# Optimization experiments

Hardware: AMD Instinct MI355X
Metric: run time of the kernel (lower is better)

Reference implementation:

```python
import jax, jax.numpy as jnp
import numpy as np
from jax import lax

B, T, C = 256, 128, 512
HID, HOR = 1024, 96
THR = 1.0


def setup_inputs() -> dict:
    key = jax.random.key(0)
    ks = jax.random.split(key, 6)
    x = jax.random.normal(ks[0], (B, T, C), dtype=jnp.float32)
    # fc1: Linear(C -> HID), PyTorch layout [out, in]
    W1 = jax.random.normal(ks[1], (HID, C), dtype=jnp.float32) / np.sqrt(C)
    b1 = jax.random.normal(ks[2], (HID,), dtype=jnp.float32) * 0.01
    # head: Linear(HID -> HOR)
    Wh = jax.random.normal(ks[3], (HOR, HID), dtype=jnp.float32) / np.sqrt(HID)
    bh = jax.random.normal(ks[4], (HOR,), dtype=jnp.float32) * 0.01
    beta = jnp.float32(0.9)  # learnable leak (snntorch Leaky, learn_beta=True)
    return {"x": x, "W1": W1, "b1": b1, "Wh": Wh, "bh": bh, "beta": beta}


def reference(x, W1, b1, Wh, bh, beta):
    # Precompute all fc1 projections as one batched GEMM: [B,T,HID]
    proj = jnp.einsum("btc,hc->bth", x, W1) + b1
    beta_c = jnp.clip(beta, 0.0, 1.0)

    def step(mem, inp):
        # snntorch Leaky, reset_mechanism='subtract': reset based on PREVIOUS mem
        reset = (mem > THR).astype(mem.dtype)  # detached in snntorch
        mem_new = beta_c * mem + inp - reset * THR
        return mem_new, None

    mem0 = jnp.zeros((x.shape[0], W1.shape[0]), dtype=x.dtype)
    mem_T, _ = lax.scan(step, mem0, jnp.moveaxis(proj, 1, 0))  # scan over T
    return mem_T @ Wh.T + bh  # [B, HOR]
```

## Files before the change

kernel.cpp:

```cpp
#include <hip/hip_runtime.h>

#define TT 128
#define CC 512
#define HIDN 1024
#define HORN 96
#define NB 256
#define BM 128
#define BN 256
#define BK 32
#define NSTAGE 16

typedef _Float16 f16x8 __attribute__((ext_vector_type(8)));
typedef _Float16 f16x4 __attribute__((ext_vector_type(4)));
typedef float f32x16 __attribute__((ext_vector_type(16)));

#define BUFSZ 49152
#define WOFF  16384
#define SMEM_BYTES 98304

__device__ __forceinline__ void cvt_split(const float4 v, f16x4* hi, f16x4* lo) {
    auto h01 = __builtin_amdgcn_cvt_pkrtz(v.x, v.y);
    auto h23 = __builtin_amdgcn_cvt_pkrtz(v.z, v.w);
    auto l01 = __builtin_amdgcn_cvt_pkrtz(v.x - (float)h01.x, v.y - (float)h01.y);
    auto l23 = __builtin_amdgcn_cvt_pkrtz(v.z - (float)h23.x, v.w - (float)h23.y);
    *hi = (f16x4){(_Float16)h01.x, (_Float16)h01.y, (_Float16)h23.x, (_Float16)h23.y};
    *lo = (f16x4){(_Float16)l01.x, (_Float16)l01.y, (_Float16)l23.x, (_Float16)l23.y};
}

__device__ __forceinline__ void cvt_split8(const float4 f0, const float4 f1,
                                           f16x8* hi, f16x8* lo) {
    auto h0 = __builtin_amdgcn_cvt_pkrtz(f0.x, f0.y);
    auto h1 = __builtin_amdgcn_cvt_pkrtz(f0.z, f0.w);
    auto h2 = __builtin_amdgcn_cvt_pkrtz(f1.x, f1.y);
    auto h3 = __builtin_amdgcn_cvt_pkrtz(f1.z, f1.w);
    auto l0 = __builtin_amdgcn_cvt_pkrtz(f0.x - (float)h0.x, f0.y - (float)h0.y);
    auto l1 = __builtin_amdgcn_cvt_pkrtz(f0.z - (float)h1.x, f0.w - (float)h1.y);
    auto l2 = __builtin_amdgcn_cvt_pkrtz(f1.x - (float)h2.x, f1.y - (float)h2.y);
    auto l3 = __builtin_amdgcn_cvt_pkrtz(f1.z - (float)h3.x, f1.w - (float)h3.y);
    *hi = (f16x8){(_Float16)h0.x, (_Float16)h0.y, (_Float16)h1.x, (_Float16)h1.y,
                  (_Float16)h2.x, (_Float16)h2.y, (_Float16)h3.x, (_Float16)h3.y};
    *lo = (f16x8){(_Float16)l0.x, (_Float16)l0.y, (_Float16)l1.x, (_Float16)l1.y,
                  (_Float16)l2.x, (_Float16)l2.y, (_Float16)l3.x, (_Float16)l3.y};
}

__device__ __forceinline__ void gload16(const void* g, void* l) {
    __builtin_amdgcn_global_load_lds(
        (const __attribute__((address_space(1))) unsigned int*)g,
        (__attribute__((address_space(3))) unsigned int*)l, 16, 0, 0);
}

__global__ void __launch_bounds__(256)
snn_cvtw(const float* __restrict__ W1, f16x4* __restrict__ whi, f16x4* __restrict__ wlo,
         const float* __restrict__ bh, float* __restrict__ out)
{
    const int i = blockIdx.x * 256 + threadIdx.x;
    const float4 v = ((const float4*)W1)[i];
    f16x4 hi, lo;
    cvt_split(v, &hi, &lo);
    whi[i] = hi;
    wlo[i] = lo;
    if (i < NB * HORN) out[i] = bh[i % HORN];
}

__global__ void __launch_bounds__(512, 1)
snn_proj_scan(const float* __restrict__ x, const _Float16* __restrict__ whi_g,
              const _Float16* __restrict__ wlo_g, const float* __restrict__ b1,
              const float* __restrict__ betap, float* __restrict__ memT)
{
    __shared__ __align__(16) char smem[SMEM_BYTES];

    const int tid  = threadIdx.x;
    const int lane = tid & 63;
    const int wid  = tid >> 6;
    const int wm = wid >> 2, wn = wid & 3;
    const int g2 = lane >> 5, lr = lane & 31;
    const int am = lr & 7;

    const int lid = blockIdx.x;
    const int idx = lid >> 3;
    const int b     = ((lid & 7) << 5) + (idx >> 2);
    const int hbase = (idx & 3) * BN;

    const int rr = lane >> 3, pp = lane & 7;
    const int uu = pp ^ rr;
    const char* xgc = (const char*)(x + (size_t)b * TT * CC);
    const char* xsrc0 = xgc + (size_t)(16 * wid + rr) * 2048 + uu * 16;
    const char* xsrc1 = xgc + (size_t)(16 * wid + 8 + rr) * 2048 + uu * 16;
    const char* wbase = (uu < 4) ? (const char*)whi_g : (const char*)wlo_g;
    const char* wsrc0 = wbase + (size_t)(hbase + 32 * wid + rr) * 1024 + (uu & 3) * 16;
    const char* wsrc1 = wsrc0 + 8 * 1024;
    const char* wsrc2 = wsrc0 + 16 * 1024;
    const char* wsrc3 = wsrc0 + 24 * 1024;

    const int arow0 = (wm * 64 + lr) * 128;
    const int arow1 = arow0 + 32 * 128;
    const int brow0 = WOFF + (wn * 64 + lr) * 128;
    const int brow1 = brow0 + 32 * 128;

    f32x16 acc00 = {}, acc01 = {}, acc10 = {}, acc11 = {};

#define STAGE_LOADS(S, BB) { \
        gload16(xsrc0 + (S) * 128, smem + (BB) + (2 * wid) * 1024); \
        gload16(xsrc1 + (S) * 128, smem + (BB) + (2 * wid + 1) * 1024); \
        gload16(wsrc0 + (S) * 64,  smem + (BB) + WOFF + (4 * wid) * 1024); \
        gload16(wsrc1 + (S) * 64,  smem + (BB) + WOFF + (4 * wid + 1) * 1024); \
        gload16(wsrc2 + (S) * 64,  smem + (BB) + WOFF + (4 * wid + 2) * 1024); \
        gload16(wsrc3 + (S) * 64,  smem + (BB) + WOFF + (4 * wid + 3) * 1024); }

#define KSTEP(CUR, KS) { \
        const int ua16 = (((KS) * 4 + g2 * 2) ^ am) << 4; \
        const int ub16 = (((KS) * 2 + g2) ^ am) << 4; \
        const float4 a00 = *(const float4*)(smem + (CUR) + arow0 + ua16); \
        const float4 a01 = *(const float4*)(smem + (CUR) + arow0 + (ua16 ^ 16)); \
        const float4 a10 = *(const float4*)(smem + (CUR) + arow1 + ua16); \
        const float4 a11 = *(const float4*)(smem + (CUR) + arow1 + (ua16 ^ 16)); \
        const f16x8 bh0 = *(const f16x8*)(smem + (CUR) + brow0 + ub16); \
        const f16x8 bl0 = *(const f16x8*)(smem + (CUR) + brow0 + (ub16 ^ 64)); \
        const f16x8 bh1 = *(const f16x8*)(smem + (CUR) + brow1 + ub16); \
        const f16x8 bl1 = *(const f16x8*)(smem + (CUR) + brow1 + (ub16 ^ 64)); \
        f16x8 ah0, al0, ah1, al1; \
        cvt_split8(a00, a01, &ah0, &al0); \
        cvt_split8(a10, a11, &ah1, &al1); \
        acc00 = __builtin_amdgcn_mfma_f32_32x32x16_f16(ah0, bh0, acc00, 0, 0, 0); \
        acc01 = __builtin_amdgcn_mfma_f32_32x32x16_f16(ah0, bh1, acc01, 0, 0, 0); \
        acc10 = __builtin_amdgcn_mfma_f32_32x32x16_f16(ah1, bh0, acc10, 0, 0, 0); \
        acc11 = __builtin_amdgcn_mfma_f32_32x32x16_f16(ah1, bh1, acc11, 0, 0, 0); \
        acc00 = __builtin_amdgcn_mfma_f32_32x32x16_f16(ah0, bl0, acc00, 0, 0, 0); \
        acc01 = __builtin_amdgcn_mfma_f32_32x32x16_f16(ah0, bl1, acc01, 0, 0, 0); \
        acc10 = __builtin_amdgcn_mfma_f32_32x32x16_f16(ah1, bl0, acc10, 0, 0, 0); \
        acc11 = __builtin_amdgcn_mfma_f32_32x32x16_f16(ah1, bl1, acc11, 0, 0, 0); \
        acc00 = __builtin_amdgcn_mfma_f32_32x32x16_f16(al0, bh0, acc00, 0, 0, 0); \
        acc01 = __builtin_amdgcn_mfma_f32_32x32x16_f16(al0, bh1, acc01, 0, 0, 0); \
        acc10 = __builtin_amdgcn_mfma_f32_32x32x16_f16(al1, bh0, acc10, 0, 0, 0); \
        acc11 = __builtin_amdgcn_mfma_f32_32x32x16_f16(al1, bh1, acc11, 0, 0, 0); }

    STAGE_LOADS(0, 0)
    asm volatile("s_waitcnt vmcnt(0)" ::: "memory");
    __builtin_amdgcn_s_barrier();

#pragma unroll
    for (int s = 0; s < NSTAGE; ++s) {
        const int cur = (s & 1) ? BUFSZ : 0;
        const int nxt = (s & 1) ? 0 : BUFSZ;
        if (s + 1 < NSTAGE) STAGE_LOADS(s + 1, nxt)
        __builtin_amdgcn_sched_barrier(0);
        __builtin_amdgcn_s_setprio(1);
        KSTEP(cur, 0)
        KSTEP(cur, 1)
        __builtin_amdgcn_s_setprio(0);
        asm volatile("s_waitcnt vmcnt(0)" ::: "memory");
        __builtin_amdgcn_s_barrier();
    }
#undef KSTEP
#undef STAGE_LOADS

#define ST_ACC(A, a, bb, wl) { \
        const int row = (wl) * 64 + (bb) * 32 + lr; \
        const int sb  = wm * 16 + (a) * 8 + g2; \
        const int rs  = row & 31; \
        char* rb = smem + row * 512; \
        *(float4*)(rb + (((sb + 0) ^ rs) * 16)) = make_float4(A[0],  A[1],  A[2],  A[3]);  \
        *(float4*)(rb + (((sb + 2) ^ rs) * 16)) = make_float4(A[4],  A[5],  A[6],  A[7]);  \
        *(float4*)(rb + (((sb + 4) ^ rs) * 16)) = make_float4(A[8],  A[9],  A[10], A[11]); \
        *(float4*)(rb + (((sb + 6) ^ rs) * 16)) = make_float4(A[12], A[13], A[14], A[15]); }

    const float beta_c = fminf(fmaxf(betap[0], 0.0f), 1.0f);

#pragma unroll
    for (int half = 0; half < 2; ++half) {
        if ((wn >> 1) == half) {
            const int wl = wn & 1;
            ST_ACC(acc00, 0, 0, wl)
            ST_ACC(acc01, 0, 1, wl)
            ST_ACC(acc10, 1, 0, wl)
            ST_ACC(acc11, 1, 1, wl)
        }
        __syncthreads();
        if (tid < 128) {
            const int hg = hbase + half * 128 + tid;
            const float b1h = b1[hg];
            const char* rb = smem + tid * 512;
            const int rs = tid & 31;
            float mem = 0.0f;
#pragma unroll
            for (int q = 0; q < 32; ++q) {
                const float4 v = *(const float4*)(rb + ((q ^ rs) * 16));
                float reset;
                reset = (mem > 1.0f) ? 1.0f : 0.0f; mem = beta_c * mem + (v.x + b1h) - reset;
                reset = (mem > 1.0f) ? 1.0f : 0.0f; mem = beta_c * mem + (v.y + b1h) - reset;
                reset = (mem > 1.0f) ? 1.0f : 0.0f; mem = beta_c * mem + (v.z + b1h) - reset;
                reset = (mem > 1.0f) ? 1.0f : 0.0f; mem = beta_c * mem + (v.w + b1h) - reset;
            }
            memT[(size_t)b * HIDN + hg] = mem;
        }
        __syncthreads();
    }
#undef ST_ACC
}

__global__ void __launch_bounds__(256)
snn_head(const float* __restrict__ memT, const float* __restrict__ Wh,
         float* __restrict__ out)
{
    __shared__ __align__(16) float ms[16][64];
    __shared__ __align__(16) float ws[HORN][64];
    const int tid = threadIdx.x;
    const int kc = blockIdx.x, bg = blockIdx.y;
    const int kof = kc * 64;

    {
        const int row = tid >> 4, c4 = tid & 15;
        *(float4*)&ms[row][c4 * 4] =
            *(const float4*)(memT + (size_t)(bg * 16 + row) * HIDN + kof + c4 * 4);
    }
#pragma unroll
    for (int r = 0; r < 6; ++r) {
        const int q = r * 256 + tid;
        const int row = q >> 4, c4 = q & 15;
        *(float4*)&ws[row][c4 * 4] =
            *(const float4*)(Wh + (size_t)row * HIDN + kof + c4 * 4);
    }
    __syncthreads();

#pragma unroll
    for (int r = 0; r < 6; ++r) {
        const int p = r * 256 + tid;
        const int bb = p / HORN, o = p % HORN;
        const float4* mv = (const float4*)&ms[bb][0];
        const float4* wv = (const float4*)&ws[o][0];
        float a = 0.0f;
#pragma unroll
        for (int q = 0; q < 16; ++q) {
            const float4 w = wv[q];
            const float4 m = mv[q];
            a = fmaf(w.x, m.x, fmaf(w.y, m.y, fmaf(w.z, m.z, fmaf(w.w, m.w, a))));
        }
        atomicAdd(out + (size_t)(bg * 16 + bb) * HORN + o, a);
    }
}

extern "C" void kernel_launch(void* const* d_in, const int* in_sizes, int n_in,
                              void* d_out, int out_size, void* d_ws, size_t ws_size,
                              hipStream_t stream)
{
    (void)in_sizes; (void)n_in; (void)out_size; (void)ws_size;
    const float* x    = (const float*)d_in[0];
    const float* W1   = (const float*)d_in[1];
    const float* b1   = (const float*)d_in[2];
    const float* Wh   = (const float*)d_in[3];
    const float* bh   = (const float*)d_in[4];
    const float* beta = (const float*)d_in[5];

    char* ws = (char*)d_ws;
    _Float16* whi  = (_Float16*)(ws);
    _Float16* wlo  = (_Float16*)(ws + (1 << 20));
    float*    memT = (float*)(ws + (2 << 20));
    float*    out  = (float*)d_out;

    snn_cvtw<<<512, 256, 0, stream>>>(W1, (f16x4*)whi, (f16x4*)wlo, bh, out);
    snn_proj_scan<<<1024, 512, 0, stream>>>(x, whi, wlo, b1, beta, memT);
    snn_head<<<dim3(16, 16), 256, 0, stream>>>(memT, Wh, out);
}
```

Measured before the change: 232.4 us.

## Enlarge projection tile to two batches per block with interleaved loads

Each block now computes a 256x256 tile covering two batch rows instead of a 128x256 tile for one. That halves the grid and doubles the MFMA work per wave (8 accumulators). Each W1 stage loaded into LDS is reused across twice as many x rows, which cuts global weight traffic. The K loop now issues the next stage's loads inside the first phase, with barriers between the LDS reads and the MFMA blocks, and launch bounds ask for 2 blocks per CU. The 128 KB LDS footprint and higher register pressure may block the intended two-block occupancy, and there are fewer blocks to spread across CUs.

```diff
diff --git a/kernel.cpp b/kernel.cpp
--- a/kernel.cpp
+++ b/kernel.cpp
@@ -5,18 +5,16 @@
 #define HIDN 1024
 #define HORN 96
 #define NB 256
-#define BM 128
-#define BN 256
-#define BK 32
-#define NSTAGE 16
+#define NTILE 16
 
 typedef _Float16 f16x8 __attribute__((ext_vector_type(8)));
 typedef _Float16 f16x4 __attribute__((ext_vector_type(4)));
 typedef float f32x16 __attribute__((ext_vector_type(16)));
 
-#define BUFSZ 49152
-#define WOFF  16384
-#define SMEM_BYTES 98304
+#define XB 0
+#define WB 32768
+#define BUFSZ 65536
+#define SMEM_BYTES 131072
 
 __device__ __forceinline__ void cvt_split(const float4 v, f16x4* hi, f16x4* lo) {
     auto h01 = __builtin_amdgcn_cvt_pkrtz(v.x, v.y);
@@ -62,7 +60,9 @@
     if (i < NB * HORN) out[i] = bh[i % HORN];
 }
 
-__global__ void __launch_bounds__(512, 1)
+#define MF(A, B, C) C = __builtin_amdgcn_mfma_f32_32x32x16_f16(A, B, C, 0, 0, 0)
+
+__global__ void __launch_bounds__(512, 2)
 snn_proj_scan(const float* __restrict__ x, const _Float16* __restrict__ whi_g,
               const _Float16* __restrict__ wlo_g, const float* __restrict__ b1,
               const float* __restrict__ betap, float* __restrict__ memT)
@@ -72,91 +72,103 @@
     const int tid  = threadIdx.x;
     const int lane = tid & 63;
     const int wid  = tid >> 6;
-    const int wm = wid >> 2, wn = wid & 3;
+    const int wm   = wid >> 2;
+    const int wn   = wid & 3;
     const int g2 = lane >> 5, lr = lane & 31;
     const int am = lr & 7;
 
     const int lid = blockIdx.x;
     const int idx = lid >> 3;
-    const int b     = ((lid & 7) << 5) + (idx >> 2);
-    const int hbase = (idx & 3) * BN;
+    const int bp    = (lid & 7) * 16 + (idx >> 2);
+    const int hbase = (idx & 3) * 256;
+
+    const char* xg = (const char*)x + (size_t)bp * 256 * 2048;
 
     const int rr = lane >> 3, pp = lane & 7;
     const int uu = pp ^ rr;
-    const char* xgc = (const char*)(x + (size_t)b * TT * CC);
-    const char* xsrc0 = xgc + (size_t)(16 * wid + rr) * 2048 + uu * 16;
-    const char* xsrc1 = xgc + (size_t)(16 * wid + 8 + rr) * 2048 + uu * 16;
-    const char* wbase = (uu < 4) ? (const char*)whi_g : (const char*)wlo_g;
-    const char* wsrc0 = wbase + (size_t)(hbase + 32 * wid + rr) * 1024 + (uu & 3) * 16;
-    const char* wsrc1 = wsrc0 + 8 * 1024;
-    const char* wsrc2 = wsrc0 + 16 * 1024;
-    const char* wsrc3 = wsrc0 + 24 * 1024;
-
-    const int arow0 = (wm * 64 + lr) * 128;
-    const int arow1 = arow0 + 32 * 128;
-    const int brow0 = WOFF + (wn * 64 + lr) * 128;
-    const int brow1 = brow0 + 32 * 128;
+    const char* xsrc = xg + (size_t)(32 * wid + rr) * 2048 + uu * 16;
+    const char* wbs  = (uu < 4) ? (const char*)whi_g : (const char*)wlo_g;
+    const char* wsrc = wbs + (size_t)(hbase + 32 * wid + rr) * 1024 + (uu & 3) * 16;
+
+    const int arow = (wm * 128 + lr) * 128;
+    const int brow = WB + (wn * 64 + lr) * 128;
 
     f32x16 acc00 = {}, acc01 = {}, acc10 = {}, acc11 = {};
-
-#define STAGE_LOADS(S, BB) { \
-        gload16(xsrc0 + (S) * 128, smem + (BB) + (2 * wid) * 1024); \
-        gload16(xsrc1 + (S) * 128, smem + (BB) + (2 * wid + 1) * 1024); \
-        gload16(wsrc0 + (S) * 64,  smem + (BB) + WOFF + (4 * wid) * 1024); \
-        gload16(wsrc1 + (S) * 64,  smem + (BB) + WOFF + (4 * wid + 1) * 1024); \
-        gload16(wsrc2 + (S) * 64,  smem + (BB) + WOFF + (4 * wid + 2) * 1024); \
-        gload16(wsrc3 + (S) * 64,  smem + (BB) + WOFF + (4 * wid + 3) * 1024); }
-
-#define KSTEP(CUR, KS) { \
-        const int ua16 = (((KS) * 4 + g2 * 2) ^ am) << 4; \
-        const int ub16 = (((KS) * 2 + g2) ^ am) << 4; \
-        const float4 a00 = *(const float4*)(smem + (CUR) + arow0 + ua16); \
-        const float4 a01 = *(const float4*)(smem + (CUR) + arow0 + (ua16 ^ 16)); \
-        const float4 a10 = *(const float4*)(smem + (CUR) + arow1 + ua16); \
-        const float4 a11 = *(const float4*)(smem + (CUR) + arow1 + (ua16 ^ 16)); \
-        const f16x8 bh0 = *(const f16x8*)(smem + (CUR) + brow0 + ub16); \
-        const f16x8 bl0 = *(const f16x8*)(smem + (CUR) + brow0 + (ub16 ^ 64)); \
-        const f16x8 bh1 = *(const f16x8*)(smem + (CUR) + brow1 + ub16); \
-        const f16x8 bl1 = *(const f16x8*)(smem + (CUR) + brow1 + (ub16 ^ 64)); \
-        f16x8 ah0, al0, ah1, al1; \
-        cvt_split8(a00, a01, &ah0, &al0); \
-        cvt_split8(a10, a11, &ah1, &al1); \
-        acc00 = __builtin_amdgcn_mfma_f32_32x32x16_f16(ah0, bh0, acc00, 0, 0, 0); \
-        acc01 = __builtin_amdgcn_mfma_f32_32x32x16_f16(ah0, bh1, acc01, 0, 0, 0); \
-        acc10 = __builtin_amdgcn_mfma_f32_32x32x16_f16(ah1, bh0, acc10, 0, 0, 0); \
-        acc11 = __builtin_amdgcn_mfma_f32_32x32x16_f16(ah1, bh1, acc11, 0, 0, 0); \
-        acc00 = __builtin_amdgcn_mfma_f32_32x32x16_f16(ah0, bl0, acc00, 0, 0, 0); \
-        acc01 = __builtin_amdgcn_mfma_f32_32x32x16_f16(ah0, bl1, acc01, 0, 0, 0); \
-        acc10 = __builtin_amdgcn_mfma_f32_32x32x16_f16(ah1, bl0, acc10, 0, 0, 0); \
-        acc11 = __builtin_amdgcn_mfma_f32_32x32x16_f16(ah1, bl1, acc11, 0, 0, 0); \
-        acc00 = __builtin_amdgcn_mfma_f32_32x32x16_f16(al0, bh0, acc00, 0, 0, 0); \
-        acc01 = __builtin_amdgcn_mfma_f32_32x32x16_f16(al0, bh1, acc01, 0, 0, 0); \
-        acc10 = __builtin_amdgcn_mfma_f32_32x32x16_f16(al1, bh0, acc10, 0, 0, 0); \
-        acc11 = __builtin_amdgcn_mfma_f32_32x32x16_f16(al1, bh1, acc11, 0, 0, 0); }
-
-    STAGE_LOADS(0, 0)
+    f32x16 acc20 = {}, acc21 = {}, acc30 = {}, acc31 = {};
+
+#define STAGE(S, BB) { \
+        _Pragma("unroll") \
+        for (int i = 0; i < 4; ++i) { \
+            gload16(xsrc + (size_t)i * (8 * 2048) + (S) * 128, \
+                    smem + (BB) + XB + (4 * wid + i) * 1024); \
+            gload16(wsrc + (size_t)i * (8 * 1024) + (S) * 64, \
+                    smem + (BB) + WB + (4 * wid + i) * 1024); \
+        } }
+
+#define PHASE(CUR, KS, ...) { \
+        __VA_ARGS__ \
+        const int ub = (((KS) * 2 + g2) ^ am) << 4; \
+        const f16x8 bh0 = *(const f16x8*)(smem + (CUR) + brow + 0 * 4096 + ub); \
+        const f16x8 bl0 = *(const f16x8*)(smem + (CUR) + brow + 0 * 4096 + (ub ^ 64)); \
+        const f16x8 bh1 = *(const f16x8*)(smem + (CUR) + brow + 1 * 4096 + ub); \
+        const f16x8 bl1 = *(const f16x8*)(smem + (CUR) + brow + 1 * 4096 + (ub ^ 64)); \
+        const int ua = (((KS) * 4 + g2 * 2) ^ am) << 4; \
+        f16x8 ah0, al0, ah1, al1, ah2, al2, ah3, al3; \
+        { float4 r0 = *(const float4*)(smem + (CUR) + arow + 0 * 4096 + ua); \
+          float4 r1 = *(const float4*)(smem + (CUR) + arow + 0 * 4096 + (ua ^ 16)); \
+          cvt_split8(r0, r1, &ah0, &al0); } \
+        { float4 r0 = *(const float4*)(smem + (CUR) + arow + 1 * 4096 + ua); \
+          float4 r1 = *(const float4*)(smem + (CUR) + arow + 1 * 4096 + (ua ^ 16)); \
+          cvt_split8(r0, r1, &ah1, &al1); } \
+        { float4 r0 = *(const float4*)(smem + (CUR) + arow + 2 * 4096 + ua); \
+          float4 r1 = *(const float4*)(smem + (CUR) + arow + 2 * 4096 + (ua ^ 16)); \
+          cvt_split8(r0, r1, &ah2, &al2); } \
+        { float4 r0 = *(const float4*)(smem + (CUR) + arow + 3 * 4096 + ua); \
+          float4 r1 = *(const float4*)(smem + (CUR) + arow + 3 * 4096 + (ua ^ 16)); \
+          cvt_split8(r0, r1, &ah3, &al3); } \
+        __builtin_amdgcn_s_barrier(); \
+        asm volatile("s_waitcnt lgkmcnt(0)" ::: "memory"); \
+        __builtin_amdgcn_sched_barrier(0); \
+        __builtin_amdgcn_s_setprio(1); \
+        MF(ah0, bh0, acc00); MF(ah0, bh1, acc01); \
+        MF(ah1, bh0, acc10); MF(ah1, bh1, acc11); \
+        MF(ah2, bh0, acc20); MF(ah2, bh1, acc21); \
+        MF(ah3, bh0, acc30); MF(ah3, bh1, acc31); \
+        MF(ah0, bl0, acc00); MF(ah0, bl1, acc01); \
+        MF(ah1, bl0, acc10); MF(ah1, bl1, acc11); \
+        MF(ah2, bl0, acc20); MF(ah2, bl1, acc21); \
+        MF(ah3, bl0, acc30); MF(ah3, bl1, acc31); \
+        MF(al0, bh0, acc00); MF(al0, bh1, acc01); \
+        MF(al1, bh0, acc10); MF(al1, bh1, acc11); \
+        MF(al2, bh0, acc20); MF(al2, bh1, acc21); \
+        MF(al3, bh0, acc30); MF(al3, bh1, acc31); \
+        __builtin_amdgcn_s_setprio(0); \
+    }
+
+    STAGE(0, 0)
     asm volatile("s_waitcnt vmcnt(0)" ::: "memory");
     __builtin_amdgcn_s_barrier();
 
-#pragma unroll
-    for (int s = 0; s < NSTAGE; ++s) {
+#pragma unroll 2
+    for (int s = 0; s < NTILE; ++s) {
         const int cur = (s & 1) ? BUFSZ : 0;
         const int nxt = (s & 1) ? 0 : BUFSZ;
-        if (s + 1 < NSTAGE) STAGE_LOADS(s + 1, nxt)
-        __builtin_amdgcn_sched_barrier(0);
-        __builtin_amdgcn_s_setprio(1);
-        KSTEP(cur, 0)
-        KSTEP(cur, 1)
-        __builtin_amdgcn_s_setprio(0);
+        if (s + 1 < NTILE) {
+            PHASE(cur, 0, STAGE(s + 1, nxt))
+        } else {
+            PHASE(cur, 0, )
+        }
+        __builtin_amdgcn_s_barrier();
+        PHASE(cur, 1, )
         asm volatile("s_waitcnt vmcnt(0)" ::: "memory");
         __builtin_amdgcn_s_barrier();
     }
-#undef KSTEP
-#undef STAGE_LOADS
-
-#define ST_ACC(A, a, bb, wl) { \
-        const int row = (wl) * 64 + (bb) * 32 + lr; \
-        const int sb  = wm * 16 + (a) * 8 + g2; \
+#undef PHASE
+#undef STAGE
+
+#define ST_ACC(A, m, n) { \
+        const int row = wn * 64 + (n) * 32 + lr; \
+        const int sb  = (m) * 8 + g2; \
         const int rs  = row & 31; \
         char* rb = smem + row * 512; \
         *(float4*)(rb + (((sb + 0) ^ rs) * 16)) = make_float4(A[0],  A[1],  A[2],  A[3]);  \
@@ -167,17 +179,16 @@
     const float beta_c = fminf(fmaxf(betap[0], 0.0f), 1.0f);
 
 #pragma unroll
-    for (int half = 0; half < 2; ++half) {
-        if ((wn >> 1) == half) {
-            const int wl = wn & 1;
-            ST_ACC(acc00, 0, 0, wl)
-            ST_ACC(acc01, 0, 1, wl)
-            ST_ACC(acc10, 1, 0, wl)
-            ST_ACC(acc11, 1, 1, wl)
+    for (int bb = 0; bb < 2; ++bb) {
+        if (wm == bb) {
+            ST_ACC(acc00, 0, 0) ST_ACC(acc01, 0, 1)
+            ST_ACC(acc10, 1, 0) ST_ACC(acc11, 1, 1)
+            ST_ACC(acc20, 2, 0) ST_ACC(acc21, 2, 1)
+            ST_ACC(acc30, 3, 0) ST_ACC(acc31, 3, 1)
         }
         __syncthreads();
-        if (tid < 128) {
-            const int hg = hbase + half * 128 + tid;
+        if (tid < 256) {
+            const int hg = hbase + tid;
             const float b1h = b1[hg];
             const char* rb = smem + tid * 512;
             const int rs = tid & 31;
@@ -191,7 +202,7 @@
                 reset = (mem > 1.0f) ? 1.0f : 0.0f; mem = beta_c * mem + (v.z + b1h) - reset;
                 reset = (mem > 1.0f) ? 1.0f : 0.0f; mem = beta_c * mem + (v.w + b1h) - reset;
             }
-            memT[(size_t)b * HIDN + hg] = mem;
+            memT[(size_t)(bp * 2 + bb) * HIDN + hg] = mem;
         }
         __syncthreads();
     }
@@ -258,6 +269,6 @@
     float*    out  = (float*)d_out;
 
     snn_cvtw<<<512, 256, 0, stream>>>(W1, (f16x4*)whi, (f16x4*)wlo, bh, out);
-    snn_proj_scan<<<1024, 512, 0, stream>>>(x, whi, wlo, b1, beta, memT);
+    snn_proj_scan<<<512, 512, 0, stream>>>(x, whi, wlo, b1, beta, memT);
     snn_head<<<dim3(16, 16), 256, 0, stream>>>(memT, Wh, out);
 }
```

New measurement: 724.4 us. +211.7%, slower.
